# Performance work log

Measured on AMD Instinct MI355X. Metric: run time of the kernel, lower is better.

Reference implementation:

```python
import jax, jax.numpy as jnp
import numpy as np

B, S, H = 2, 2048, 1024
NH, NKV, HD = 16, 4, 64

def setup_inputs() -> dict:
    key = jax.random.key(0)
    k1, k2, k3, k4, k5 = jax.random.split(key, 5)
    return {
        "hidden_states": jax.random.normal(k1, (B, S, H), dtype=jnp.float32),
        "attention_mask": jnp.ones((B, S), dtype=jnp.int32),
        "wq": jax.random.normal(k2, (H, NH * HD), dtype=jnp.float32) * 0.02,
        "wk": jax.random.normal(k3, (H, NKV * HD), dtype=jnp.float32) * 0.02,
        "wv": jax.random.normal(k4, (H, NKV * HD), dtype=jnp.float32) * 0.02,
        "wo": jax.random.normal(k5, (NH * HD, 1), dtype=jnp.float32) * 0.02,
    }

def reference(hidden_states, attention_mask, wq, wk, wv, wo):
    bsz, seq_len, _ = hidden_states.shape
    n_rep = NH // NKV
    # projections -> (b, h, s, d)
    q = (hidden_states @ wq).reshape(bsz, seq_len, NH, HD).transpose(0, 2, 1, 3)
    k = (hidden_states @ wk).reshape(bsz, seq_len, NKV, HD).transpose(0, 2, 1, 3)
    v = (hidden_states @ wv).reshape(bsz, seq_len, NKV, HD).transpose(0, 2, 1, 3)
    # repeat_kv == repeat_interleave along head axis
    k = jnp.repeat(k, n_rep, axis=1)
    v = jnp.repeat(v, n_rep, axis=1)
    scores = jnp.einsum('bhqd,bhkd->bhqk', q, k) / np.sqrt(HD).astype(np.float32)
    mask = attention_mask[:, None, None, :]  # (b,1,1,k)
    scores = jnp.where(mask == 0, jnp.float32(-jnp.inf), scores)
    attn = jax.nn.softmax(scores, axis=-1)
    out = jnp.einsum('bhqk,bhkd->bqhd', attn, v).reshape(bsz, seq_len, NH * HD)
    return out @ wo  # (b, s, 1)
```

## Files before the change

kernel.cpp:

```cpp
#include <hip/hip_runtime.h>
#include <stdint.h>


typedef __bf16 bf16x8 __attribute__((ext_vector_type(8)));
typedef float f32x4 __attribute__((ext_vector_type(4)));
typedef float f32x2 __attribute__((ext_vector_type(2)));

__device__ inline unsigned short f2bf(float f) {
    unsigned int u = __builtin_bit_cast(unsigned int, f);
    u += 0x7fff + ((u >> 16) & 1);
    return (unsigned short)(u >> 16);
}
__device__ inline bf16x8 ldfrag(const unsigned short* p) {
    uint4 v = *(const uint4*)p;
    return __builtin_bit_cast(bf16x8, v);
}
__device__ inline void gl2lds16(const unsigned short* g, unsigned short* l) {
    __builtin_amdgcn_global_load_lds(
        (const __attribute__((address_space(1))) void*)g,
        (__attribute__((address_space(3))) void*)l, 16, 0, 0);
}

#define SCALE_Q 0.18033688011112042f

__global__ __launch_bounds__(256) void prep_kernel(
    const float* __restrict__ hs, const float* __restrict__ wq,
    const float* __restrict__ wk, const float* __restrict__ wv,
    const float* __restrict__ wo,
    unsigned short* __restrict__ hs_bf, unsigned short* __restrict__ wT)
{
    int bid = blockIdx.x, tid = threadIdx.x;
    if (bid < 4096) {
        int u = bid * 256 + tid;
        float4 v = ((const float4*)hs)[u];
        ushort4 o;
        o.x = f2bf(v.x); o.y = f2bf(v.y); o.z = f2bf(v.z); o.w = f2bf(v.w);
        ((ushort4*)hs_bf)[u] = o;
    } else if (bid < 4416) {
        __shared__ float tile[64 * 65];
        int t = bid - 4096;
        int ntile = t / 16, ctile = t % 16;
        int nb = ntile * 64, cb = ctile * 64;
        int tx = tid & 63, ty = tid >> 6;
        for (int i = 0; i < 16; i++) {
            int cl = i * 4 + ty;
            int n = nb + tx;
            float v = (n < 1024) ? wq[(cb + cl) * 1024 + n] * SCALE_Q
                                 : wk[(cb + cl) * 256 + (n - 1024)];
            tile[cl * 65 + tx] = v;
        }
        __syncthreads();
        for (int i = 0; i < 16; i++) {
            int nl = i * 4 + ty;
            wT[(nb + nl) * 1024 + cb + tx] = f2bf(tile[tx * 65 + nl]);
        }
    } else {
        int u = (bid - 4416) * 256 + tid;
        int n2 = u >> 10, c = u & 1023;
        if (n2 < 16) {
            int h = n2, kv = h >> 2;
            const float* wvr = wv + c * 256 + kv * 64;
            const float* wor = wo + h * 64;
            float s = 0.f;
            #pragma unroll 8
            for (int d = 0; d < 64; d++) s += wvr[d] * wor[d];
            wT[(1280 + n2) * 1024 + c] = f2bf(s);
        } else {
            wT[(1280 + n2) * 1024 + c] = 0;
        }
    }
}

__global__ __launch_bounds__(256) void gemm_kernel(
    const unsigned short* __restrict__ hs_bf, const unsigned short* __restrict__ wT,
    unsigned short* __restrict__ Qp, unsigned short* __restrict__ Kp,
    float* __restrict__ vproj)
{
    __shared__ __align__(16) unsigned short Al[2][128 * 32];
    __shared__ __align__(16) unsigned short Bl[2][64 * 32];
    int p = blockIdx.x + 11 * blockIdx.y;
    int xcd = p & 7;
    int j = p >> 3;
    int rt = (xcd << 3) + j / 11;
    int nt = j % 11;
    int tid = threadIdx.x;
    int lane = tid & 63, w = tid >> 6;
    int l15 = lane & 15, quad = lane >> 4;
    int wm = (w >> 1) * 64, wn = (w & 1) * 32;

    f32x4 acc[4][2];
    const f32x4 zero = {0.f, 0.f, 0.f, 0.f};
    for (int i = 0; i < 4; i++) for (int j2 = 0; j2 < 2; j2++) acc[i][j2] = zero;

    int arow = nt * 128, rrow = rt * 64;
    int srowA = w * 32 + (lane >> 2);
    int srowB = w * 16 + (lane >> 2);
    int scol = (lane & 3) * 8;
    const unsigned short* ga = wT    + (size_t)(arow + srowA) * 1024 + scol;
    const unsigned short* gb = hs_bf + (size_t)(rrow + srowB) * 1024 + scol;
    int lofsA = (w * 32) * 32;
    int lofsB = (w * 16) * 32;

    gl2lds16(ga,             Al[0] + lofsA);
    gl2lds16(ga + 16 * 1024, Al[0] + lofsA + 16 * 32);
    gl2lds16(gb,             Bl[0] + lofsB);
    ga += 32; gb += 32;
    __syncthreads();

    for (int kk = 0; kk < 32; kk++) {
        int cur = kk & 1, nxt = cur ^ 1;
        if (kk < 31) {
            gl2lds16(ga,             Al[nxt] + lofsA);
            gl2lds16(ga + 16 * 1024, Al[nxt] + lofsA + 16 * 32);
            gl2lds16(gb,             Bl[nxt] + lofsB);
            ga += 32; gb += 32;
        }
        bf16x8 af[4], bfr[2];
        for (int i = 0; i < 4; i++)
            af[i]  = ldfrag(Al[cur] + (wm + i * 16 + l15) * 32 + quad * 8);
        for (int j2 = 0; j2 < 2; j2++)
            bfr[j2] = ldfrag(Bl[cur] + (wn + j2 * 16 + l15) * 32 + quad * 8);
        for (int i = 0; i < 4; i++)
            for (int j2 = 0; j2 < 2; j2++)
                acc[i][j2] = __builtin_amdgcn_mfma_f32_16x16x32_bf16(af[i], bfr[j2], acc[i][j2], 0, 0, 0);
        __syncthreads();
    }

    for (int i = 0; i < 4; i++) {
        for (int j2 = 0; j2 < 2; j2++) {
            int nw = nt * 128 + wm + i * 16 + quad * 4;
            int r  = rt * 64 + wn + j2 * 16 + l15;
            if (nt < 8) {
                ushort4 o;
                o.x = f2bf(acc[i][j2][0]); o.y = f2bf(acc[i][j2][1]);
                o.z = f2bf(acc[i][j2][2]); o.w = f2bf(acc[i][j2][3]);
                *(ushort4*)(Qp + (size_t)r * 1024 + nw) = o;
            } else if (nt < 10) {
                ushort4 o;
                o.x = f2bf(acc[i][j2][0]); o.y = f2bf(acc[i][j2][1]);
                o.z = f2bf(acc[i][j2][2]); o.w = f2bf(acc[i][j2][3]);
                *(ushort4*)(Kp + (size_t)r * 256 + (nw - 1024)) = o;
            } else {
                for (int rg = 0; rg < 4; rg++) {
                    int h = nw + rg - 1280;
                    if (h < 16)
                        vproj[((size_t)(r >> 11) * 16 + h) * 2048 + (r & 2047)] = acc[i][j2][rg];
                }
            }
        }
    }
}

__global__ __launch_bounds__(256) void attn_kernel(
    const unsigned short* __restrict__ Qp, const unsigned short* __restrict__ Kp,
    const float* __restrict__ vproj, const int* __restrict__ mask,
    float2* __restrict__ part)
{
    __shared__ __align__(16) unsigned short Kl[256 * 64];
    __shared__ __align__(16) float vpml[4 * 256];
    __shared__ __align__(16) float biasl[256];
    int qt = blockIdx.x;
    int b = blockIdx.y >> 2, kv = blockIdx.y & 3;
    int ks = blockIdx.z;
    int tid = threadIdx.x, lane = tid & 63, w = tid >> 6;
    int l15 = lane & 15, quad = lane >> 4;
    int h = kv * 4 + w;
    int k0 = ks * 256;
    int qrow0 = qt * 64;

    {
        int swz = (lane & 7) ^ ((lane >> 3) & 7);
        const unsigned short* kbase =
            Kp + (size_t)(b * 2048 + k0 + w * 64 + (lane >> 3)) * 256 + kv * 64 + swz * 8;
        unsigned short* ldst = Kl + (w * 64) * 64;
        #pragma unroll
        for (int j = 0; j < 8; j++)
            gl2lds16(kbase + (size_t)(j * 8) * 256, ldst + j * 8 * 64);
    }

    bf16x8 qf[4][2];
    for (int qs = 0; qs < 4; qs++) {
        const unsigned short* qp =
            Qp + (size_t)(b * 2048 + qrow0 + qs * 16 + l15) * 1024 + h * 64 + quad * 8;
        qf[qs][0] = ldfrag(qp);
        qf[qs][1] = ldfrag(qp + 32);
    }

    {
        int h2 = tid >> 6, kk = (tid & 63) * 4;
        *(float4*)(vpml + h2 * 256 + kk) =
            *(const float4*)(vproj + ((size_t)b * 16 + kv * 4 + h2) * 2048 + k0 + kk);
    }
    if (tid < 64) {
        int4 mm = *(const int4*)(mask + b * 2048 + k0 + tid * 4);
        float4 bb;
        bb.x = mm.x ? 0.f : -30000.f;
        bb.y = mm.y ? 0.f : -30000.f;
        bb.z = mm.z ? 0.f : -30000.f;
        bb.w = mm.w ? 0.f : -30000.f;
        *(float4*)(biasl + tid * 4) = bb;
    }
    __syncthreads();

    f32x2 nd[4];
    const f32x2 zero2 = {0.f, 0.f};
    for (int qs = 0; qs < 4; qs++) nd[qs] = zero2;

    for (int t8 = 0; t8 < 16; t8++) {
        int r0 = t8 * 16 + l15;
        int rx = r0 & 7;
        bf16x8 a0 = ldfrag(Kl + r0 * 64 + ((quad ^ rx) * 8));
        bf16x8 a1 = ldfrag(Kl + r0 * 64 + (((quad ^ rx) ^ 4) * 8));
        f32x4 vpm4 = *(const f32x4*)(vpml + w * 256 + t8 * 16 + quad * 4);
        f32x4 c4   = *(const f32x4*)(biasl + t8 * 16 + quad * 4);
        for (int qs = 0; qs < 4; qs++) {
            __builtin_amdgcn_s_setprio(1);
            f32x4 d = __builtin_amdgcn_mfma_f32_16x16x32_bf16(a0, qf[qs][0], c4, 0, 0, 0);
            d = __builtin_amdgcn_mfma_f32_16x16x32_bf16(a1, qf[qs][1], d, 0, 0, 0);
            __builtin_amdgcn_s_setprio(0);
            for (int r = 0; r < 4; r++) {
                float e = __builtin_amdgcn_exp2f(d[r]);
                f32x2 m = {vpm4[r], 1.0f};
                nd[qs] += m * e;
            }
        }
    }
    for (int qs = 0; qs < 4; qs++) {
        float n = nd[qs][0], dd = nd[qs][1];
        n += __shfl_xor(n, 16);  n += __shfl_xor(n, 32);
        dd += __shfl_xor(dd, 16); dd += __shfl_xor(dd, 32);
        if (quad == 0) {
            int q = qrow0 + qs * 16 + l15;
            part[((size_t)(b * 2048 + q) * 16 + h) * 8 + ks] = make_float2(n, dd);
        }
    }
}

__global__ __launch_bounds__(256) void combine_kernel(
    const float2* __restrict__ part, float* __restrict__ out)
{
    int wid = (blockIdx.x * 256 + threadIdx.x) >> 6;
    int lane = threadIdx.x & 63;
    const float2* base = part + (size_t)wid * 128;
    float2 p0 = base[lane];
    float2 p1 = base[64 + lane];
    for (int m = 1; m <= 4; m <<= 1) {
        p0.x += __shfl_xor(p0.x, m); p0.y += __shfl_xor(p0.y, m);
        p1.x += __shfl_xor(p1.x, m); p1.y += __shfl_xor(p1.y, m);
    }
    float v = p0.x / p0.y + p1.x / p1.y;
    for (int m = 8; m <= 32; m <<= 1) v += __shfl_xor(v, m);
    if (lane == 0) out[wid] = v;
}

extern "C" void kernel_launch(void* const* d_in, const int* in_sizes, int n_in,
                              void* d_out, int out_size, void* d_ws, size_t ws_size,
                              hipStream_t stream)
{
    const float* hs  = (const float*)d_in[0];
    const int* mask  = (const int*)d_in[1];
    const float* wq  = (const float*)d_in[2];
    const float* wk  = (const float*)d_in[3];
    const float* wv  = (const float*)d_in[4];
    const float* wo  = (const float*)d_in[5];

    char* ws = (char*)d_ws;
    unsigned short* hs_bf = (unsigned short*)ws;
    unsigned short* wT    = (unsigned short*)(ws + 8388608);
    unsigned short* Qp    = (unsigned short*)(ws + 11272192);
    unsigned short* Kp    = (unsigned short*)(ws + 19660800);
    float* vproj          = (float*)(ws + 21757952);
    float2* part          = (float2*)(ws + 22020096);

    prep_kernel<<<4928, 256, 0, stream>>>(hs, wq, wk, wv, wo, hs_bf, wT);
    gemm_kernel<<<dim3(11, 64), 256, 0, stream>>>(hs_bf, wT, Qp, Kp, vproj);
    attn_kernel<<<dim3(32, 8, 8), 256, 0, stream>>>(Qp, Kp, vproj, mask, part);
    combine_kernel<<<1024, 256, 0, stream>>>(part, (float*)d_out);
}
```

Before: 140.0 us.

## Fuse hidden-state bf16 conversion into GEMM and combine into attention

The separate fp32-to-bf16 pass over hidden states is removed. The GEMM now loads fp32 rows straight into LDS through an XOR-swizzled layout and converts them to bf16 while building the MFMA fragments. The final combine kernel is folded into the attention kernel: a per-tile atomic counter lets the last finishing split-K block reduce the partials. Together these drop one full read/write of the hidden states plus two launches, at the cost of twice the B-tile LDS traffic, conversion ALU work in the GEMM inner loop, and an atomic/fence tail in attention.

```diff
diff --git a/kernel.cpp b/kernel.cpp
--- a/kernel.cpp
+++ b/kernel.cpp
@@ -15,7 +15,7 @@
     uint4 v = *(const uint4*)p;
     return __builtin_bit_cast(bf16x8, v);
 }
-__device__ inline void gl2lds16(const unsigned short* g, unsigned short* l) {
+__device__ inline void gl2lds16(const void* g, void* l) {
     __builtin_amdgcn_global_load_lds(
         (const __attribute__((address_space(1))) void*)g,
         (__attribute__((address_space(3))) void*)l, 16, 0, 0);
@@ -24,21 +24,14 @@
 #define SCALE_Q 0.18033688011112042f
 
 __global__ __launch_bounds__(256) void prep_kernel(
-    const float* __restrict__ hs, const float* __restrict__ wq,
-    const float* __restrict__ wk, const float* __restrict__ wv,
-    const float* __restrict__ wo,
-    unsigned short* __restrict__ hs_bf, unsigned short* __restrict__ wT)
+    const float* __restrict__ wq, const float* __restrict__ wk,
+    const float* __restrict__ wv, const float* __restrict__ wo,
+    unsigned short* __restrict__ wT, int* __restrict__ cnt)
 {
     int bid = blockIdx.x, tid = threadIdx.x;
-    if (bid < 4096) {
-        int u = bid * 256 + tid;
-        float4 v = ((const float4*)hs)[u];
-        ushort4 o;
-        o.x = f2bf(v.x); o.y = f2bf(v.y); o.z = f2bf(v.z); o.w = f2bf(v.w);
-        ((ushort4*)hs_bf)[u] = o;
-    } else if (bid < 4416) {
+    if (bid < 320) {
         __shared__ float tile[64 * 65];
-        int t = bid - 4096;
+        int t = bid;
         int ntile = t / 16, ctile = t % 16;
         int nb = ntile * 64, cb = ctile * 64;
         int tx = tid & 63, ty = tid >> 6;
@@ -55,7 +48,8 @@
             wT[(nb + nl) * 1024 + cb + tx] = f2bf(tile[tx * 65 + nl]);
         }
     } else {
-        int u = (bid - 4416) * 256 + tid;
+        if (bid == 320 && tid < 64) cnt[tid] = 0;
+        int u = (bid - 320) * 256 + tid;
         int n2 = u >> 10, c = u & 1023;
         if (n2 < 16) {
             int h = n2, kv = h >> 2;
@@ -72,12 +66,12 @@
 }
 
 __global__ __launch_bounds__(256) void gemm_kernel(
-    const unsigned short* __restrict__ hs_bf, const unsigned short* __restrict__ wT,
+    const float* __restrict__ hs, const unsigned short* __restrict__ wT,
     unsigned short* __restrict__ Qp, unsigned short* __restrict__ Kp,
     float* __restrict__ vproj)
 {
     __shared__ __align__(16) unsigned short Al[2][128 * 32];
-    __shared__ __align__(16) unsigned short Bl[2][64 * 32];
+    __shared__ __align__(16) float Blf[2][64 * 32];
     int p = blockIdx.x + 11 * blockIdx.y;
     int xcd = p & 7;
     int j = p >> 3;
@@ -94,16 +88,18 @@
 
     int arow = nt * 128, rrow = rt * 64;
     int srowA = w * 32 + (lane >> 2);
-    int srowB = w * 16 + (lane >> 2);
-    int scol = (lane & 3) * 8;
-    const unsigned short* ga = wT    + (size_t)(arow + srowA) * 1024 + scol;
-    const unsigned short* gb = hs_bf + (size_t)(rrow + srowB) * 1024 + scol;
+    int scolA = (lane & 3) * 8;
+    const unsigned short* ga = wT + (size_t)(arow + srowA) * 1024 + scolA;
     int lofsA = (w * 32) * 32;
+    int rB = lane >> 3, chB = lane & 7;
+    int swzB = chB ^ rB;
+    const float* gb = hs + (size_t)(rrow + w * 16 + rB) * 1024 + swzB * 4;
     int lofsB = (w * 16) * 32;
 
     gl2lds16(ga,             Al[0] + lofsA);
     gl2lds16(ga + 16 * 1024, Al[0] + lofsA + 16 * 32);
-    gl2lds16(gb,             Bl[0] + lofsB);
+    gl2lds16(gb,             Blf[0] + lofsB);
+    gl2lds16(gb + 8 * 1024,  Blf[0] + lofsB + 8 * 32);
     ga += 32; gb += 32;
     __syncthreads();
 
@@ -112,14 +108,26 @@
         if (kk < 31) {
             gl2lds16(ga,             Al[nxt] + lofsA);
             gl2lds16(ga + 16 * 1024, Al[nxt] + lofsA + 16 * 32);
-            gl2lds16(gb,             Bl[nxt] + lofsB);
+            gl2lds16(gb,             Blf[nxt] + lofsB);
+            gl2lds16(gb + 8 * 1024,  Blf[nxt] + lofsB + 8 * 32);
             ga += 32; gb += 32;
         }
         bf16x8 af[4], bfr[2];
         for (int i = 0; i < 4; i++)
-            af[i]  = ldfrag(Al[cur] + (wm + i * 16 + l15) * 32 + quad * 8);
-        for (int j2 = 0; j2 < 2; j2++)
-            bfr[j2] = ldfrag(Bl[cur] + (wn + j2 * 16 + l15) * 32 + quad * 8);
+            af[i] = ldfrag(Al[cur] + (wm + i * 16 + l15) * 32 + quad * 8);
+        for (int j2 = 0; j2 < 2; j2++) {
+            int r = wn + j2 * 16 + l15;
+            int rx = r & 7;
+            const float* rowp = Blf[cur] + r * 32;
+            float4 f0 = *(const float4*)(rowp + (((quad * 2)     ^ rx) << 2));
+            float4 f1 = *(const float4*)(rowp + (((quad * 2 + 1) ^ rx) << 2));
+            bf16x8 bb;
+            bb[0] = (__bf16)f0.x; bb[1] = (__bf16)f0.y;
+            bb[2] = (__bf16)f0.z; bb[3] = (__bf16)f0.w;
+            bb[4] = (__bf16)f1.x; bb[5] = (__bf16)f1.y;
+            bb[6] = (__bf16)f1.z; bb[7] = (__bf16)f1.w;
+            bfr[j2] = bb;
+        }
         for (int i = 0; i < 4; i++)
             for (int j2 = 0; j2 < 2; j2++)
                 acc[i][j2] = __builtin_amdgcn_mfma_f32_16x16x32_bf16(af[i], bfr[j2], acc[i][j2], 0, 0, 0);
@@ -154,11 +162,12 @@
 __global__ __launch_bounds__(256) void attn_kernel(
     const unsigned short* __restrict__ Qp, const unsigned short* __restrict__ Kp,
     const float* __restrict__ vproj, const int* __restrict__ mask,
-    float2* __restrict__ part)
+    float2* __restrict__ part, int* __restrict__ cnt, float* __restrict__ out)
 {
     __shared__ __align__(16) unsigned short Kl[256 * 64];
     __shared__ __align__(16) float vpml[4 * 256];
     __shared__ __align__(16) float biasl[256];
+    __shared__ int lastflag;
     int qt = blockIdx.x;
     int b = blockIdx.y >> 2, kv = blockIdx.y & 3;
     int ks = blockIdx.z;
@@ -234,23 +243,33 @@
             part[((size_t)(b * 2048 + q) * 16 + h) * 8 + ks] = make_float2(n, dd);
         }
     }
-}
-
-__global__ __launch_bounds__(256) void combine_kernel(
-    const float2* __restrict__ part, float* __restrict__ out)
-{
-    int wid = (blockIdx.x * 256 + threadIdx.x) >> 6;
-    int lane = threadIdx.x & 63;
-    const float2* base = part + (size_t)wid * 128;
-    float2 p0 = base[lane];
-    float2 p1 = base[64 + lane];
-    for (int m = 1; m <= 4; m <<= 1) {
-        p0.x += __shfl_xor(p0.x, m); p0.y += __shfl_xor(p0.y, m);
-        p1.x += __shfl_xor(p1.x, m); p1.y += __shfl_xor(p1.y, m);
-    }
-    float v = p0.x / p0.y + p1.x / p1.y;
-    for (int m = 8; m <= 32; m <<= 1) v += __shfl_xor(v, m);
-    if (lane == 0) out[wid] = v;
+
+    __threadfence();
+    __syncthreads();
+    if (tid == 0)
+        lastflag = (atomicAdd(cnt + (b * 32 + qt), 1) == 31);
+    __syncthreads();
+    if (lastflag) {
+        __threadfence();
+        for (int i = 0; i < 16; i++) {
+            int q = qrow0 + w * 16 + i;
+            const unsigned long long* pb =
+                (const unsigned long long*)(part + (size_t)(b * 2048 + q) * 128);
+            unsigned long long u0 = __hip_atomic_load(pb + lane,
+                __ATOMIC_RELAXED, __HIP_MEMORY_SCOPE_AGENT);
+            unsigned long long u1 = __hip_atomic_load(pb + 64 + lane,
+                __ATOMIC_RELAXED, __HIP_MEMORY_SCOPE_AGENT);
+            float2 p0 = __builtin_bit_cast(float2, u0);
+            float2 p1 = __builtin_bit_cast(float2, u1);
+            for (int m = 1; m <= 4; m <<= 1) {
+                p0.x += __shfl_xor(p0.x, m); p0.y += __shfl_xor(p0.y, m);
+                p1.x += __shfl_xor(p1.x, m); p1.y += __shfl_xor(p1.y, m);
+            }
+            float v = p0.x / p0.y + p1.x / p1.y;
+            for (int m = 8; m <= 32; m <<= 1) v += __shfl_xor(v, m);
+            if (lane == 0) out[b * 2048 + q] = v;
+        }
+    }
 }
 
 extern "C" void kernel_launch(void* const* d_in, const int* in_sizes, int n_in,
@@ -265,15 +284,14 @@
     const float* wo  = (const float*)d_in[5];
 
     char* ws = (char*)d_ws;
-    unsigned short* hs_bf = (unsigned short*)ws;
-    unsigned short* wT    = (unsigned short*)(ws + 8388608);
-    unsigned short* Qp    = (unsigned short*)(ws + 11272192);
-    unsigned short* Kp    = (unsigned short*)(ws + 19660800);
-    float* vproj          = (float*)(ws + 21757952);
-    float2* part          = (float2*)(ws + 22020096);
-
-    prep_kernel<<<4928, 256, 0, stream>>>(hs, wq, wk, wv, wo, hs_bf, wT);
-    gemm_kernel<<<dim3(11, 64), 256, 0, stream>>>(hs_bf, wT, Qp, Kp, vproj);
-    attn_kernel<<<dim3(32, 8, 8), 256, 0, stream>>>(Qp, Kp, vproj, mask, part);
-    combine_kernel<<<1024, 256, 0, stream>>>(part, (float*)d_out);
-}
+    unsigned short* wT = (unsigned short*)ws;
+    unsigned short* Qp = (unsigned short*)(ws + 2883584);
+    unsigned short* Kp = (unsigned short*)(ws + 11272192);
+    float* vproj       = (float*)(ws + 13369344);
+    float2* part       = (float2*)(ws + 13631488);
+    int* cnt           = (int*)(ws + 17825792);
+
+    prep_kernel<<<832, 256, 0, stream>>>(wq, wk, wv, wo, wT, cnt);
+    gemm_kernel<<<dim3(11, 64), 256, 0, stream>>>(hs, wT, Qp, Kp, vproj);
+    attn_kernel<<<dim3(32, 8, 8), 256, 0, stream>>>(Qp, Kp, vproj, mask, part, cnt, (float*)d_out);
+}
```

Measured after the change: 381.3 us. 172% more time.
